# Kernel tuning notes

Measured on AMD Instinct MI355X. Metric: run time of the kernel, lower is better.

## Reference

```python
import jax, jax.numpy as jnp
import numpy as np

B, N, D, H = 2, 512, 128, 8
DK = D // H

def setup_inputs() -> dict:
    key = jax.random.key(0)
    ks = jax.random.split(key, 7)
    s = lambda fan_in: 1.0 / np.sqrt(fan_in)
    return {
        "n": jax.random.normal(ks[0], (B, N, D), dtype=jnp.float32),
        "e": jax.random.normal(ks[1], (B, N, N, D), dtype=jnp.float32),
        "W_qkv": jax.random.normal(ks[2], (D, 3 * D), dtype=jnp.float32) * s(D),
        "O_n": jax.random.normal(ks[3], (D, D), dtype=jnp.float32) * s(D),
        "W_g": jax.random.normal(ks[4], (D, H), dtype=jnp.float32) * s(D),
        "W_e": jax.random.normal(ks[5], (D, H), dtype=jnp.float32) * s(D),
        "O_e": jax.random.normal(ks[6], (H, D), dtype=jnp.float32) * s(H),
    }

def reference(n, e, W_qkv, O_n, W_g, W_e, O_e):
    b, nn_, d = n.shape
    # QKV projection -> [B, H, N, DK] each
    qkv = (n @ W_qkv).reshape(b, nn_, 3, H, DK)
    qkv = jnp.transpose(qkv, (2, 0, 3, 1, 4))
    Q, K, V = qkv[0], qkv[1], qkv[2]
    # Edge bias and gate: [B, H, N, N]
    E = jnp.einsum('bnmd,dh->bhnm', e, W_e)
    G = jax.nn.sigmoid(jnp.einsum('bnmd,dh->bhnm', e, W_g))
    dyn_cent = jnp.log1p(G.sum(-1))  # [B, H, N]
    # Attention scores with clamp + edge bias
    A_raw = jnp.einsum('bhnd,bhmd->bhnm', Q, K) * (DK ** -0.5)
    A_raw = jnp.clip(A_raw, -5.0, 5.0)
    _E = A_raw + E
    A = jax.nn.softmax(_E, axis=-1)
    # Weighted values, rescaled by dynamic centrality
    _V = jnp.einsum('bhnm,bhmd->bhnd', A, V) * dyn_cent[..., None]
    n_out = jnp.transpose(_V, (0, 2, 1, 3)).reshape(b, nn_, d) @ O_n
    e_out = jnp.einsum('bhnm,hd->bnmd', _E, O_e)
    return n_out, e_out
```

## Files before the change

kernel.cpp:

```cpp
#include <hip/hip_runtime.h>
#include <math.h>

#define BB 2
#define NN 512
#define DD 128
#define HH 8
#define DKK 16
#define TR 64
#define NT (NN / TR)
#define ETS 516

typedef __attribute__((ext_vector_type(8))) short short8;
typedef __attribute__((ext_vector_type(4))) float f32x4;

__device__ __forceinline__ float dot4(float4 a, float4 b) {
    return a.x*b.x + a.y*b.y + a.z*b.z + a.w*b.w;
}
__device__ __forceinline__ unsigned pk_bf16(float a, float b) {
    unsigned ua = __float_as_uint(a), ub = __float_as_uint(b);
    ua = (ua + 0x7FFFu + ((ua >> 16) & 1u)) >> 16;
    ub = (ub + 0x7FFFu + ((ub >> 16) & 1u)) >> 16;
    return ua | (ub << 16);
}

__global__ __launch_bounds__(128)
void qkv_kernel(const float* __restrict__ n_in,
                const float* __restrict__ W_qkv,
                const float* __restrict__ W_g,
                const float* __restrict__ W_e,
                float* __restrict__ Qw, float* __restrict__ Kw,
                float* __restrict__ Vw, float* __restrict__ WegT)
{
    const int bid = blockIdx.x;
    if (bid >= BB * NN) {
        const int col = bid - BB * NN;
        const int t = threadIdx.x;
        WegT[col * DD + t] = (col < 8) ? W_e[t * HH + col]
                                       : W_g[t * HH + (col - 8)];
        return;
    }
    __shared__ float nrow[DD];
    const int bn = bid;
    const int b  = bn >> 9;
    const int nr = bn & 511;
    const int t  = threadIdx.x;
    nrow[t] = n_in[(size_t)bn * DD + t];
    __syncthreads();
    const int h = t >> 4, dk = t & 15;
    const size_t dst = ((size_t)(b * HH + h) * NN + nr) * DKK + dk;
    float accq = 0.f, acck = 0.f, accv = 0.f;
    #pragma unroll 8
    for (int d = 0; d < DD; ++d) {
        const float nv = nrow[d];
        const float* wr = W_qkv + (size_t)d * 3 * DD;
        accq += nv * wr[t];
        acck += nv * wr[t + 128];
        accv += nv * wr[t + 256];
    }
    Qw[dst] = accq;
    Kw[dst] = acck;
    Vw[dst] = accv;
}

__global__ __attribute__((amdgpu_flat_work_group_size(512, 512),
                          amdgpu_waves_per_eu(4, 8)))
void eg_kernel(const float* __restrict__ e,
               const float* __restrict__ WegT,
               const float* __restrict__ O_e,
               const float* __restrict__ Qw,
               const float* __restrict__ Kw,
               const float* __restrict__ Vw,
               const float* __restrict__ O_n,
               float* __restrict__ n_out,
               float* __restrict__ e_out)
{
    __shared__ __align__(16) uint4 ebuf4[TR * 16];
    __shared__ __align__(16) float ET[HH * ETS];
    __shared__ float Gred[64];
    __shared__ float dc[HH];
    __shared__ __align__(16) float vout[DD];

    const int t    = threadIdx.x;
    const int bn   = blockIdx.x;
    const int b    = bn >> 9;
    const int nr   = bn & 511;
    const int wq   = t >> 6;
    const int lane = t & 63;
    const int c    = lane & 15;
    const int mq   = lane >> 4;
    const int wgrp = wq & 3;
    const int wpar = wq >> 2;
    const int c4o  = t & 31;
    const int mr0  = t >> 5;

    const float4* __restrict__ e4    = (const float4*)e + (size_t)bn * NN * 32;
    const float4* __restrict__ WegT4 = (const float4*)WegT;

    short8 wB[4];
    #pragma unroll
    for (int kb = 0; kb < 4; ++kb) {
        const float4 wa = WegT4[c * 32 + kb * 8 + mq * 2];
        const float4 wb = WegT4[c * 32 + kb * 8 + mq * 2 + 1];
        uint4 u;
        u.x = pk_bf16(wa.x, wa.y); u.y = pk_bf16(wa.z, wa.w);
        u.z = pk_bf16(wb.x, wb.y); u.w = pk_bf16(wb.z, wb.w);
        wB[kb] = *(short8*)&u;
    }

    float4 pa0, pb0, pa1, pb1;

    #define STAGE_LOAD(tile)                                                  \
    {                                                                         \
        const float4* __restrict__ sp = e4 + (size_t)(tile) * 2048 + 2 * t;   \
        pa0 = sp[0];    pb0 = sp[1];                                          \
        pa1 = sp[1024]; pb1 = sp[1025];                                       \
    }
    #define STAGE_WRITE(U, A, B)                                              \
    {                                                                         \
        const int u_ = (U), ms = u_ >> 4, ck = u_ & 15;                       \
        uint4 x;                                                              \
        x.x = pk_bf16(A.x, A.y); x.y = pk_bf16(A.z, A.w);                     \
        x.z = pk_bf16(B.x, B.y); x.w = pk_bf16(B.z, B.w);                     \
        ebuf4[ms * 16 + (ck ^ (ms & 15))] = x;                                \
    }
    #define STAGE_WRITE_ALL()                                                 \
    {                                                                         \
        STAGE_WRITE(t, pa0, pb0); STAGE_WRITE(t + 512, pa1, pb1);             \
    }

    float ga0 = 0.f, ga1 = 0.f, ga2 = 0.f, ga3 = 0.f;

    STAGE_LOAD(0);

    {
        const int h = wq;
        const float4* __restrict__ qp =
            (const float4*)(Qw + ((size_t)(b * HH + h) * NN + nr) * DKK);
        const float4 q0 = qp[0], q1 = qp[1], q2 = qp[2], q3 = qp[3];
        const float4* __restrict__ kb =
            (const float4*)(Kw + ((size_t)(b * HH + h) * NN) * DKK);
        #pragma unroll
        for (int k = 0; k < 8; ++k) {
            const int m = k * 64 + lane;
            float s = dot4(q0, kb[m * 4 + 0]) + dot4(q1, kb[m * 4 + 1])
                    + dot4(q2, kb[m * 4 + 2]) + dot4(q3, kb[m * 4 + 3]);
            s *= 0.25f;
            ET[h * ETS + m] = fminf(5.f, fmaxf(-5.f, s));
        }
    }

    STAGE_WRITE_ALL();
    asm volatile("s_waitcnt lgkmcnt(0)" ::: "memory");
    __builtin_amdgcn_s_barrier();

    #pragma unroll
    for (int tt = 0; tt < NT; ++tt) {
        if (tt + 1 < NT) STAGE_LOAD(tt + 1);

        if (wpar == (tt & 1)) {
            const int mrow = wgrp * 16 + c;
            f32x4 acc = {0.f, 0.f, 0.f, 0.f};
            #pragma unroll
            for (int kb = 0; kb < 4; ++kb) {
                const int ck = kb * 4 + mq;
                uint4 av = ebuf4[mrow * 16 + (ck ^ (mrow & 15))];
                acc = __builtin_amdgcn_mfma_f32_16x16x32_bf16(
                          *(short8*)&av, wB[kb], acc, 0, 0, 0);
            }
            const int mloc = tt * TR + wgrp * 16 + mq * 4;
            if (c < 8) {
                float4 prev = *(float4*)&ET[c * ETS + mloc];
                prev.x += acc[0]; prev.y += acc[1];
                prev.z += acc[2]; prev.w += acc[3];
                *(float4*)&ET[c * ETS + mloc] = prev;
            } else {
                ga0 += 1.f / (1.f + __expf(-acc[0]));
                ga1 += 1.f / (1.f + __expf(-acc[1]));
                ga2 += 1.f / (1.f + __expf(-acc[2]));
                ga3 += 1.f / (1.f + __expf(-acc[3]));
            }
        }
        asm volatile("s_waitcnt lgkmcnt(0)" ::: "memory");
        __builtin_amdgcn_s_barrier();

        if (tt + 1 < NT) {
            STAGE_WRITE_ALL();
            asm volatile("s_waitcnt lgkmcnt(0)" ::: "memory");
            __builtin_amdgcn_s_barrier();
        }
    }

    if (c >= 8) {
        float s = ga0 + ga1 + ga2 + ga3;
        s += __shfl_xor(s, 16, 64);
        s += __shfl_xor(s, 32, 64);
        if (lane < 16) Gred[wq * 8 + (c - 8)] = s;
    }
    __syncthreads();
    if (t < 8) {
        float s = 0.f;
        #pragma unroll
        for (int w = 0; w < 8; ++w) s += Gred[w * 8 + t];
        dc[t] = log1pf(s);
    }
    __syncthreads();

    {
        float4 oe[8];
        #pragma unroll
        for (int h = 0; h < 8; ++h)
            oe[h] = ((const float4*)O_e)[h * 32 + c4o];
        float4* __restrict__ out4 = (float4*)e_out + (size_t)bn * NN * 32;
        #pragma unroll 4
        for (int it = 0; it < 32; ++it) {
            const int m = mr0 + it * 16;
            float4 rr{0.f, 0.f, 0.f, 0.f};
            #pragma unroll
            for (int h = 0; h < 8; ++h) {
                const float ev = ET[h * ETS + m];
                rr.x += ev * oe[h].x;
                rr.y += ev * oe[h].y;
                rr.z += ev * oe[h].z;
                rr.w += ev * oe[h].w;
            }
            out4[m * 32 + c4o] = rr;
        }
    }

    {
        const int h = wq;
        float vals[8];
        float rmax = -1e30f;
        #pragma unroll
        for (int k = 0; k < 8; ++k) {
            vals[k] = ET[h * ETS + k * 64 + lane];
            rmax = fmaxf(rmax, vals[k]);
        }
        #pragma unroll
        for (int off = 32; off >= 1; off >>= 1)
            rmax = fmaxf(rmax, __shfl_xor(rmax, off, 64));
        float sum = 0.f;
        #pragma unroll
        for (int k = 0; k < 8; ++k) sum += __expf(vals[k] - rmax);
        #pragma unroll
        for (int off = 32; off >= 1; off >>= 1)
            sum += __shfl_xor(sum, off, 64);
        const float factor = dc[h] / sum;

        const int ddx = lane & 15, mg = lane >> 4;
        const float* __restrict__ vb = Vw + ((size_t)(b * HH + h) * NN) * DKK;
        float av = 0.f;
        #pragma unroll 4
        for (int m = mg; m < NN; m += 4) {
            const float p = __expf(ET[h * ETS + m] - rmax);
            av += p * vb[m * DKK + ddx];
        }
        av += __shfl_xor(av, 16, 64);
        av += __shfl_xor(av, 32, 64);
        if (mg == 0) vout[h * DKK + ddx] = av * factor;
    }
    __syncthreads();

    if (t < DD) {
        float a3 = 0.f;
        #pragma unroll 4
        for (int d = 0; d < DD; ++d) a3 += vout[d] * O_n[d * DD + t];
        n_out[(size_t)bn * DD + t] = a3;
    }
    #undef STAGE_LOAD
    #undef STAGE_WRITE
    #undef STAGE_WRITE_ALL
}

extern "C" void kernel_launch(void* const* d_in, const int* in_sizes, int n_in,
                              void* d_out, int out_size, void* d_ws, size_t ws_size,
                              hipStream_t stream)
{
    const float* n_ptr = (const float*)d_in[0];
    const float* e     = (const float*)d_in[1];
    const float* W_qkv = (const float*)d_in[2];
    const float* O_n   = (const float*)d_in[3];
    const float* W_g   = (const float*)d_in[4];
    const float* W_e   = (const float*)d_in[5];
    const float* O_e   = (const float*)d_in[6];

    float* n_out = (float*)d_out;
    float* e_out = n_out + (size_t)BB * NN * DD;

    float* Qw   = (float*)d_ws;
    float* Kw   = Qw + (size_t)BB * HH * NN * DKK;
    float* Vw   = Kw + (size_t)BB * HH * NN * DKK;
    float* WegT = Vw + (size_t)BB * HH * NN * DKK;

    qkv_kernel<<<BB * NN + 16, 128, 0, stream>>>(n_ptr, W_qkv, W_g, W_e,
                                                 Qw, Kw, Vw, WegT);
    eg_kernel<<<BB * NN, 512, 0, stream>>>(e, WegT, O_e, Qw, Kw, Vw, O_n,
                                           n_out, e_out);
}
```

Before: 164.1 us.

## Deepen e-tile prefetch to two tiles and restructure epilogue loops

The edge-tile streaming loop now keeps two register sets of prefetched e data, issuing global loads two tiles ahead instead of one, so HBM latency has more time to hide behind MFMA work. The e_out projection now reads float4 of ET and writes four consecutive rows per thread. The softmax·V step reuses the exponentials and vectorized V loads, reducing with DPP/permlane. The waves-per-EU attribute changes to 8. Costs are higher register pressure from the extra prefetch set and accumulators, which conflicts with the occupancy hint. The new e_out layout also makes each wave's stores less contiguous.

```diff
diff --git a/kernel.cpp b/kernel.cpp
--- a/kernel.cpp
+++ b/kernel.cpp
@@ -21,6 +21,39 @@
     ua = (ua + 0x7FFFu + ((ua >> 16) & 1u)) >> 16;
     ub = (ub + 0x7FFFu + ((ub >> 16) & 1u)) >> 16;
     return ua | (ub << 16);
+}
+
+template<int CTRL>
+__device__ __forceinline__ float dpp_sum(float x) {
+    return x + __int_as_float(__builtin_amdgcn_mov_dpp(
+        __float_as_int(x), CTRL, 0xF, 0xF, true));
+}
+__device__ __forceinline__ float pl16_sum(float x) {
+#if __has_builtin(__builtin_amdgcn_permlane16_swap)
+    auto p = __builtin_amdgcn_permlane16_swap(__float_as_int(x),
+                                              __float_as_int(x), false, false);
+    return __int_as_float(p[0]) + __int_as_float(p[1]);
+#else
+    return x + __shfl_xor(x, 16, 64);
+#endif
+}
+__device__ __forceinline__ float pl32_sum(float x) {
+#if __has_builtin(__builtin_amdgcn_permlane32_swap)
+    auto p = __builtin_amdgcn_permlane32_swap(__float_as_int(x),
+                                              __float_as_int(x), false, false);
+    return __int_as_float(p[0]) + __int_as_float(p[1]);
+#else
+    return x + __shfl_xor(x, 32, 64);
+#endif
+}
+__device__ __forceinline__ float red64(float x) {
+    x = dpp_sum<0xB1>(x);
+    x = dpp_sum<0x4E>(x);
+    x += __shfl_xor(x, 4, 64);
+    x += __shfl_xor(x, 8, 64);
+    x = pl16_sum(x);
+    x = pl32_sum(x);
+    return x;
 }
 
 __global__ __launch_bounds__(128)
@@ -63,7 +96,7 @@
 }
 
 __global__ __attribute__((amdgpu_flat_work_group_size(512, 512),
-                          amdgpu_waves_per_eu(4, 8)))
+                          amdgpu_waves_per_eu(8)))
 void eg_kernel(const float* __restrict__ e,
                const float* __restrict__ WegT,
                const float* __restrict__ O_e,
@@ -108,29 +141,34 @@
     }
 
     float4 pa0, pb0, pa1, pb1;
-
-    #define STAGE_LOAD(tile)                                                  \
+    float4 qa0, qb0, qa1, qb1;
+
+    #define LOAD_SET0(tile)                                                   \
     {                                                                         \
         const float4* __restrict__ sp = e4 + (size_t)(tile) * 2048 + 2 * t;   \
         pa0 = sp[0];    pb0 = sp[1];                                          \
         pa1 = sp[1024]; pb1 = sp[1025];                                       \
     }
-    #define STAGE_WRITE(U, A, B)                                              \
+    #define LOAD_SET1(tile)                                                   \
+    {                                                                         \
+        const float4* __restrict__ sp = e4 + (size_t)(tile) * 2048 + 2 * t;   \
+        qa0 = sp[0];    qb0 = sp[1];                                          \
+        qa1 = sp[1024]; qb1 = sp[1025];                                       \
+    }
+    #define STAGE_W1(U, A, Bv)                                                \
     {                                                                         \
         const int u_ = (U), ms = u_ >> 4, ck = u_ & 15;                       \
         uint4 x;                                                              \
-        x.x = pk_bf16(A.x, A.y); x.y = pk_bf16(A.z, A.w);                     \
-        x.z = pk_bf16(B.x, B.y); x.w = pk_bf16(B.z, B.w);                     \
+        x.x = pk_bf16(A.x, A.y);   x.y = pk_bf16(A.z, A.w);                   \
+        x.z = pk_bf16(Bv.x, Bv.y); x.w = pk_bf16(Bv.z, Bv.w);                 \
         ebuf4[ms * 16 + (ck ^ (ms & 15))] = x;                                \
     }
-    #define STAGE_WRITE_ALL()                                                 \
-    {                                                                         \
-        STAGE_WRITE(t, pa0, pb0); STAGE_WRITE(t + 512, pa1, pb1);             \
-    }
+    #define WRITE_SET0() { STAGE_W1(t, pa0, pb0); STAGE_W1(t + 512, pa1, pb1); }
+    #define WRITE_SET1() { STAGE_W1(t, qa0, qb0); STAGE_W1(t + 512, qa1, qb1); }
 
     float ga0 = 0.f, ga1 = 0.f, ga2 = 0.f, ga3 = 0.f;
 
-    STAGE_LOAD(0);
+    LOAD_SET0(0);
 
     {
         const int h = wq;
@@ -149,14 +187,14 @@
         }
     }
 
-    STAGE_WRITE_ALL();
+    LOAD_SET1(1);
+    WRITE_SET0();
+    LOAD_SET0(2);
     asm volatile("s_waitcnt lgkmcnt(0)" ::: "memory");
     __builtin_amdgcn_s_barrier();
 
     #pragma unroll
     for (int tt = 0; tt < NT; ++tt) {
-        if (tt + 1 < NT) STAGE_LOAD(tt + 1);
-
         if (wpar == (tt & 1)) {
             const int mrow = wgrp * 16 + c;
             f32x4 acc = {0.f, 0.f, 0.f, 0.f};
@@ -184,7 +222,13 @@
         __builtin_amdgcn_s_barrier();
 
         if (tt + 1 < NT) {
-            STAGE_WRITE_ALL();
+            if ((tt + 1) & 1) {
+                WRITE_SET1();
+                if (tt + 3 < NT) LOAD_SET1(tt + 3);
+            } else {
+                WRITE_SET0();
+                if (tt + 3 < NT) LOAD_SET0(tt + 3);
+            }
             asm volatile("s_waitcnt lgkmcnt(0)" ::: "memory");
             __builtin_amdgcn_s_barrier();
         }
@@ -211,19 +255,26 @@
         for (int h = 0; h < 8; ++h)
             oe[h] = ((const float4*)O_e)[h * 32 + c4o];
         float4* __restrict__ out4 = (float4*)e_out + (size_t)bn * NN * 32;
-        #pragma unroll 4
-        for (int it = 0; it < 32; ++it) {
-            const int m = mr0 + it * 16;
-            float4 rr{0.f, 0.f, 0.f, 0.f};
+        #pragma unroll 2
+        for (int g = 0; g < 8; ++g) {
+            const int m0 = mr0 * 32 + g * 4;
+            float4 r0{0,0,0,0}, r1{0,0,0,0}, r2{0,0,0,0}, r3{0,0,0,0};
             #pragma unroll
             for (int h = 0; h < 8; ++h) {
-                const float ev = ET[h * ETS + m];
-                rr.x += ev * oe[h].x;
-                rr.y += ev * oe[h].y;
-                rr.z += ev * oe[h].z;
-                rr.w += ev * oe[h].w;
+                const float4 ev = *(const float4*)&ET[h * ETS + m0];
+                r0.x += ev.x*oe[h].x; r0.y += ev.x*oe[h].y;
+                r0.z += ev.x*oe[h].z; r0.w += ev.x*oe[h].w;
+                r1.x += ev.y*oe[h].x; r1.y += ev.y*oe[h].y;
+                r1.z += ev.y*oe[h].z; r1.w += ev.y*oe[h].w;
+                r2.x += ev.z*oe[h].x; r2.y += ev.z*oe[h].y;
+                r2.z += ev.z*oe[h].z; r2.w += ev.z*oe[h].w;
+                r3.x += ev.w*oe[h].x; r3.y += ev.w*oe[h].y;
+                r3.z += ev.w*oe[h].z; r3.w += ev.w*oe[h].w;
             }
-            out4[m * 32 + c4o] = rr;
+            out4[(m0 + 0) * 32 + c4o] = r0;
+            out4[(m0 + 1) * 32 + c4o] = r1;
+            out4[(m0 + 2) * 32 + c4o] = r2;
+            out4[(m0 + 3) * 32 + c4o] = r3;
         }
     }
 
@@ -241,23 +292,50 @@
             rmax = fmaxf(rmax, __shfl_xor(rmax, off, 64));
         float sum = 0.f;
         #pragma unroll
-        for (int k = 0; k < 8; ++k) sum += __expf(vals[k] - rmax);
+        for (int k = 0; k < 8; ++k) {
+            vals[k] = __expf(vals[k] - rmax);
+            sum += vals[k];
+        }
         #pragma unroll
         for (int off = 32; off >= 1; off >>= 1)
             sum += __shfl_xor(sum, off, 64);
         const float factor = dc[h] / sum;
 
-        const int ddx = lane & 15, mg = lane >> 4;
-        const float* __restrict__ vb = Vw + ((size_t)(b * HH + h) * NN) * DKK;
-        float av = 0.f;
-        #pragma unroll 4
-        for (int m = mg; m < NN; m += 4) {
-            const float p = __expf(ET[h * ETS + m] - rmax);
-            av += p * vb[m * DKK + ddx];
-        }
-        av += __shfl_xor(av, 16, 64);
-        av += __shfl_xor(av, 32, 64);
-        if (mg == 0) vout[h * DKK + ddx] = av * factor;
+        const float4* __restrict__ vb4 =
+            (const float4*)(Vw + ((size_t)(b * HH + h) * NN) * DKK);
+        float4 av0{0,0,0,0}, av1{0,0,0,0}, av2{0,0,0,0}, av3{0,0,0,0};
+        #pragma unroll
+        for (int k = 0; k < 8; ++k) {
+            const int m = k * 64 + lane;
+            const float p = vals[k];
+            const float4 v0 = vb4[m * 4 + 0];
+            const float4 v1 = vb4[m * 4 + 1];
+            const float4 v2 = vb4[m * 4 + 2];
+            const float4 v3 = vb4[m * 4 + 3];
+            av0.x += p*v0.x; av0.y += p*v0.y; av0.z += p*v0.z; av0.w += p*v0.w;
+            av1.x += p*v1.x; av1.y += p*v1.y; av1.z += p*v1.z; av1.w += p*v1.w;
+            av2.x += p*v2.x; av2.y += p*v2.y; av2.z += p*v2.z; av2.w += p*v2.w;
+            av3.x += p*v3.x; av3.y += p*v3.y; av3.z += p*v3.z; av3.w += p*v3.w;
+        }
+        av0.x = red64(av0.x); av0.y = red64(av0.y);
+        av0.z = red64(av0.z); av0.w = red64(av0.w);
+        av1.x = red64(av1.x); av1.y = red64(av1.y);
+        av1.z = red64(av1.z); av1.w = red64(av1.w);
+        av2.x = red64(av2.x); av2.y = red64(av2.y);
+        av2.z = red64(av2.z); av2.w = red64(av2.w);
+        av3.x = red64(av3.x); av3.y = red64(av3.y);
+        av3.z = red64(av3.z); av3.w = red64(av3.w);
+        if (lane == 0) {
+            float* vo = &vout[h * DKK];
+            vo[0]  = av0.x * factor; vo[1]  = av0.y * factor;
+            vo[2]  = av0.z * factor; vo[3]  = av0.w * factor;
+            vo[4]  = av1.x * factor; vo[5]  = av1.y * factor;
+            vo[6]  = av1.z * factor; vo[7]  = av1.w * factor;
+            vo[8]  = av2.x * factor; vo[9]  = av2.y * factor;
+            vo[10] = av2.z * factor; vo[11] = av2.w * factor;
+            vo[12] = av3.x * factor; vo[13] = av3.y * factor;
+            vo[14] = av3.z * factor; vo[15] = av3.w * factor;
+        }
     }
     __syncthreads();
 
@@ -267,9 +345,11 @@
         for (int d = 0; d < DD; ++d) a3 += vout[d] * O_n[d * DD + t];
         n_out[(size_t)bn * DD + t] = a3;
     }
-    #undef STAGE_LOAD
-    #undef STAGE_WRITE
-    #undef STAGE_WRITE_ALL
+    #undef LOAD_SET0
+    #undef LOAD_SET1
+    #undef STAGE_W1
+    #undef WRITE_SET0
+    #undef WRITE_SET1
 }
 
 extern "C" void kernel_launch(void* const* d_in, const int* in_sizes, int n_in,
```

Result: slower. 303.7 us (+85.1%).
